# Kernel optimization log

Measured on AMD Instinct MI355X. Metric: run time of the kernel, lower is better.

The kernel has to match this reference:

```python
import jax, jax.numpy as jnp
import numpy as np

DIM = 512
HEADS = 8
HEAD_DIM = DIM // HEADS
SCALE = HEAD_DIM ** -0.5
EPS = 1e-5


def _layernorm(x, w, b):
    mu = jnp.mean(x, axis=-1, keepdims=True)
    var = jnp.mean(jnp.square(x - mu), axis=-1, keepdims=True)
    return (x - mu) * jax.lax.rsqrt(var + EPS) * w + b


def setup_inputs() -> dict:
    key = jax.random.key(0)
    ks = jax.random.split(key, 9)
    B, Hs, Ws = 8, 32, 32
    r = jax.random.normal(ks[0], (B, DIM, Hs, Ws), dtype=jnp.float32)
    z = jax.random.normal(ks[1], (B, DIM, Hs, Ws), dtype=jnp.float32)
    w = lambda k: jax.random.normal(k, (DIM, DIM), dtype=jnp.float32) * 0.02
    return {
        "r": r,
        "z": z,
        "norm_r_w": jnp.ones((DIM,), jnp.float32),
        "norm_r_b": jnp.zeros((DIM,), jnp.float32),
        "norm_z_w": jnp.ones((DIM,), jnp.float32),
        "norm_z_b": jnp.zeros((DIM,), jnp.float32),
        "Wq": w(ks[2]),  # [out, in] torch Linear convention, no bias (qkv_bias=False)
        "Wk": w(ks[3]),
        "Wv": w(ks[4]),
        "Wa": w(ks[5]),
        "Wproj": w(ks[6]),
        "bproj": jax.random.normal(ks[7], (DIM,), dtype=jnp.float32) * 0.02,
    }


def reference(r, z, norm_r_w, norm_r_b, norm_z_w, norm_z_b, Wq, Wk, Wv, Wa, Wproj, bproj):
    z_sc = z
    B, C, Hz, Wz = z.shape
    # flatten(2).permute(0,2,1): NCHW -> [B, N, C]
    rf = r.reshape(B, C, -1).transpose(0, 2, 1)  # [B, Nr, C]
    zf = z.reshape(B, C, -1).transpose(0, 2, 1)  # [B, Nz, C]
    Nr, Nz = rf.shape[1], zf.shape[1]

    rf = _layernorm(rf, norm_r_w, norm_r_b)
    zf = _layernorm(zf, norm_z_w, norm_z_b)

    def heads(x, W, N):  # torch Linear: x @ W.T, then split heads -> [B,H,N,D]
        return (x @ W.T).reshape(B, N, HEADS, HEAD_DIM).transpose(0, 2, 1, 3)

    q = heads(rf, Wq, Nr)  # [B,H,Nr,D]
    k = heads(rf, Wk, Nr)  # [B,H,Nr,D]
    v = heads(zf, Wv, Nz)  # [B,H,Nz,D]
    a = heads(zf, Wa, Nz)  # [B,H,Nz,D]

    # stage 1: softmax(k @ a^T) @ v  -> anchor-aggregated values per r-token
    attn1 = jax.nn.softmax(jnp.einsum('bhnd,bhmd->bhnm', k, a) * SCALE, axis=-1)  # [B,H,Nr,Nz]
    v1 = jnp.einsum('bhnm,bhmd->bhnd', attn1, v)  # [B,H,Nr,D]

    # stage 2: softmax(a @ q^T) @ v1 -> outputs aligned with z tokens
    attn2 = jax.nn.softmax(jnp.einsum('bhmd,bhnd->bhmn', a, q) * SCALE, axis=-1)  # [B,H,Nz,Nr]
    out = jnp.einsum('bhmn,bhnd->bhmd', attn2, v1)  # [B,H,Nz,D]

    out = out.transpose(0, 2, 1, 3).reshape(B, Nz, C)
    out = out @ Wproj.T + bproj
    out = out.transpose(0, 2, 1).reshape(B, C, Hz, Wz)
    return out + z_sc
```

## Files before the change

### kernel.cpp

```cpp
#include <hip/hip_runtime.h>
#include <hip/hip_bf16.h>
#include <stdint.h>


using bf16 = __bf16;
typedef __bf16 bf16x4 __attribute__((ext_vector_type(4)));
typedef __bf16 bf16x8 __attribute__((ext_vector_type(8)));
typedef float f32x4 __attribute__((ext_vector_type(4)));
typedef float f32x16 __attribute__((ext_vector_type(16)));

#define DIMC 512
#define NTOK 1024
#define NB 8
#define NH 8
#define HD 64

__device__ __forceinline__ void gload_lds16(const bf16* g, bf16* l) {
  __builtin_amdgcn_global_load_lds((__attribute__((address_space(1))) void*)g,
                                   (__attribute__((address_space(3))) void*)l,
                                   16, 0, 0);
}

__device__ __forceinline__ float bpermf(int srclane, float v) {
  int i = __builtin_amdgcn_ds_bpermute(srclane << 2, __builtin_bit_cast(int, v));
  return __builtin_bit_cast(float, i);
}

__device__ __forceinline__ int pkbf(float lo, float hi) {
  unsigned short a = __builtin_bit_cast(unsigned short, (bf16)lo);
  unsigned short b = __builtin_bit_cast(unsigned short, (bf16)hi);
  return (int)((unsigned)a | ((unsigned)b << 16));
}

__device__ __forceinline__ float fexp2(float x) {
  float r;
  asm("v_exp_f32 %0, %1" : "=v"(r) : "v"(x));
  return r;
}

__global__ __launch_bounds__(256) void k_ln_fused(
    const float* __restrict__ r, const float* __restrict__ z,
    const float* __restrict__ wr, const float* __restrict__ br,
    const float* __restrict__ wz, const float* __restrict__ bz,
    bf16* __restrict__ rf, bf16* __restrict__ zf) {
  __shared__ float sp[4][64], ssq[4][64];
  __shared__ float muS[64], rsS[64];
  __shared__ __align__(16) bf16 T[64 * 72];
  int n0 = blockIdx.x * 64, b = blockIdx.y, tensor = blockIdx.z;
  const float* x   = tensor ? z  : r;
  const float* w   = tensor ? wz : wr;
  const float* bia = tensor ? bz : br;
  bf16* out = tensor ? zf : rf;
  int tid = threadIdx.x;

  {
    int n = tid & 63, grp = tid >> 6;
    const float* xp = x + ((size_t)(b * DIMC + grp * 128)) * NTOK + n0 + n;
    float s = 0.f, ss = 0.f;
#pragma unroll 8
    for (int c = 0; c < 128; ++c) {
      float v = xp[(size_t)c * NTOK];
      s += v; ss += v * v;
    }
    sp[grp][n] = s; ssq[grp][n] = ss;
  }
  __syncthreads();
  if (tid < 64) {
    float s  = sp[0][tid] + sp[1][tid] + sp[2][tid] + sp[3][tid];
    float ss = ssq[0][tid] + ssq[1][tid] + ssq[2][tid] + ssq[3][tid];
    float m = s * (1.0f / DIMC);
    muS[tid] = m;
    rsS[tid] = rsqrtf(ss * (1.0f / DIMC) - m * m + 1e-5f);
  }
  __syncthreads();

  int cl = tid >> 3;
  int nl = (tid & 7) * 8;
  for (int cs = 0; cs < 8; ++cs) {
    int c0 = cs * 64;
#pragma unroll
    for (int pass = 0; pass < 2; ++pass) {
      int c = c0 + pass * 32 + cl;
      float wc = w[c], bc = bia[c];
      const float* src = x + ((size_t)(b * DIMC + c)) * NTOK + n0 + nl;
      float4 v0 = *reinterpret_cast<const float4*>(src);
      float4 v1 = *reinterpret_cast<const float4*>(src + 4);
      float vv[8] = {v0.x, v0.y, v0.z, v0.w, v1.x, v1.y, v1.z, v1.w};
#pragma unroll
      for (int j = 0; j < 8; ++j) {
        int n = nl + j;
        float val = (vv[j] - muS[n]) * rsS[n] * wc + bc;
        T[n * 72 + pass * 32 + cl] = (bf16)val;
      }
    }
    __syncthreads();
#pragma unroll
    for (int pass = 0; pass < 2; ++pass) {
      int n = pass * 32 + cl;
      bf16x8 o;
#pragma unroll
      for (int j = 0; j < 8; ++j) o[j] = T[n * 72 + nl + j];
      *reinterpret_cast<bf16x8*>(out + ((size_t)(b * NTOK + n0 + n)) * DIMC + c0 + nl) = o;
    }
    __syncthreads();
  }
}

__global__ __launch_bounds__(256) void k_cvt5(
    const float* __restrict__ W0, const float* __restrict__ W1,
    const float* __restrict__ W2, const float* __restrict__ W3,
    const float* __restrict__ W4, bf16* __restrict__ out) {
  int m = blockIdx.y;
  const float* W = (m == 0) ? W0 : (m == 1) ? W1 : (m == 2) ? W2 : (m == 3) ? W3 : W4;
  bf16* o = out + (size_t)m * DIMC * DIMC;
  int i = blockIdx.x * 256 + threadIdx.x;
  float4 v = reinterpret_cast<const float4*>(W)[i];
  bf16x4 b;
  b[0] = (bf16)v.x; b[1] = (bf16)v.y; b[2] = (bf16)v.z; b[3] = (bf16)v.w;
  *reinterpret_cast<bf16x4*>(o + (size_t)i * 4) = b;
}

template <int MODE>
__global__ __launch_bounds__(256) void k_gemm(
    const bf16* __restrict__ actA, const bf16* __restrict__ zf,
    const bf16* __restrict__ Wbf,
    void* __restrict__ outbase,
    const float* __restrict__ zres, const float* __restrict__ bproj) {
  __shared__ __align__(16) bf16 As[128 * 32];
  __shared__ __align__(16) bf16 Bs[128 * 32];
  int b = blockIdx.z;
  const bf16 *Ap, *Bp;
  int m0, n0;
  int mat = (MODE == 0) ? blockIdx.y : -1;
  if (MODE == 0 && mat < 3) {
    Ap = (mat < 2 ? actA : zf) + (size_t)b * NTOK * DIMC;
    int widx = (mat == 2) ? 3 : mat;
    Bp = Wbf + (size_t)widx * DIMC * DIMC;
    m0 = (blockIdx.x >> 2) * 128;
    n0 = (blockIdx.x & 3) * 128;
  } else {
    Ap = Wbf + (size_t)(MODE == 1 ? 4 : 2) * DIMC * DIMC;
    Bp = (MODE == 1 ? actA : zf) + (size_t)b * NTOK * DIMC;
    m0 = (blockIdx.x >> 3) * 128;
    n0 = (blockIdx.x & 7) * 128;
  }
  int tid = threadIdx.x;
  int w = tid >> 6, l = tid & 63;
  int wm = (w >> 1) * 64, wn = (w & 1) * 64;
  int lr = l & 15, lg = l >> 4;
  int srow = l >> 2;
  int scol = (l & 3) * 8;
  f32x4 acc[4][4] = {};

  for (int kt = 0; kt < 16; ++kt) {
    int k0 = kt * 32;
#pragma unroll
    for (int q = 0; q < 2; ++q) {
      int rowA = w * 32 + q * 16 + srow;
      gload_lds16(Ap + (size_t)(m0 + rowA) * DIMC + k0 + scol, &As[(w * 32 + q * 16) * 32]);
      gload_lds16(Bp + (size_t)(n0 + rowA) * DIMC + k0 + scol, &Bs[(w * 32 + q * 16) * 32]);
    }
    __syncthreads();
    bf16x8 af[4], bfr[4];
#pragma unroll
    for (int i = 0; i < 4; ++i)
      af[i] = *reinterpret_cast<const bf16x8*>(&As[(wm + 16 * i + lr) * 32 + lg * 8]);
#pragma unroll
    for (int j = 0; j < 4; ++j)
      bfr[j] = *reinterpret_cast<const bf16x8*>(&Bs[(wn + 16 * j + lr) * 32 + lg * 8]);
#pragma unroll
    for (int i = 0; i < 4; ++i)
#pragma unroll
      for (int j = 0; j < 4; ++j)
        acc[i][j] = __builtin_amdgcn_mfma_f32_16x16x32_bf16(af[i], bfr[j], acc[i][j], 0, 0, 0);
    __syncthreads();
  }

  const size_t SLOT = (size_t)NB * NH * NTOK * HD;
#pragma unroll
  for (int i = 0; i < 4; ++i) {
#pragma unroll
    for (int j = 0; j < 4; ++j) {
#pragma unroll
      for (int rr = 0; rr < 4; ++rr) {
        int mm = m0 + wm + 16 * i + lg * 4 + rr;
        int nn = n0 + wn + 16 * j + lr;
        if (MODE == 0 && mat < 3) {
          bf16* outp = (bf16*)outbase + (size_t)mat * SLOT + (size_t)b * (NH * NTOK * HD);
          outp[((size_t)((nn >> 6) * NTOK + mm)) * HD + (nn & 63)] = (bf16)acc[i][j][rr];
        } else if (MODE == 0) {
          bf16* outp = (bf16*)outbase + 3 * SLOT + (size_t)b * DIMC * NTOK;
          outp[(size_t)mm * NTOK + nn] = (bf16)acc[i][j][rr];
        } else {
          float* outp = (float*)outbase + (size_t)b * DIMC * NTOK;
          const float* zp = zres + (size_t)b * DIMC * NTOK;
          size_t idx = (size_t)mm * NTOK + nn;
          outp[idx] = acc[i][j][rr] + bproj[mm] + zp[idx];
        }
      }
    }
  }
}

__global__ __launch_bounds__(128) void k_flash7(
    const bf16* __restrict__ Qp, const bf16* __restrict__ Kp,
    const bf16* __restrict__ Vtp, bf16* __restrict__ Op, int out_mode) {
  __shared__ __align__(16) bf16 smem[16384];
  int tid = threadIdx.x;
  int w = tid >> 6, l = tid & 63;
  int hl = l >> 5, ln31 = l & 31;
  int id = blockIdx.x;
  int qt = (id >> 3) & 15;
  int bh = ((id & 7) << 3) | (id >> 7);
  int q0 = qt * 64;
  const bf16* Qb = Qp + (size_t)bh * NTOK * HD;
  const bf16* Kb = Kp + (size_t)bh * NTOK * HD;
  const bf16* Vb = Vtp + (size_t)bh * HD * NTOK;

  const float QS = 0.125f * 1.44269504088896340736f;
  bf16x8 qf[4];
  int qrow = q0 + w * 32 + ln31;
#pragma unroll
  for (int s = 0; s < 4; ++s) {
    bf16x8 raw = *reinterpret_cast<const bf16x8*>(Qb + (size_t)qrow * 64 + 16 * s + 8 * hl);
#pragma unroll
    for (int j = 0; j < 8; ++j) qf[s][j] = (bf16)((float)raw[j] * QS);
  }

  int fco = hl * 512 + ln31 * 8;

#pragma unroll
  for (int gg = 0; gg < 4; ++gg) {
    int g = 4 * w + gg;
    int koff = (g >> 1) * 16 + (g & 1) * 8;
    gload_lds16(Kb + (size_t)l * 64 + koff, &smem[g * 512]);
    gload_lds16(Vb + (size_t)l * 1024 + koff, &smem[4096 + g * 512]);
  }

  float l_run = 0.f;
  f32x16 of0{}, of1{};

#pragma unroll 1
  for (int kt = 0; kt < 16; ++kt) {
    __syncthreads();
    int buf = (kt & 1) ? 8192 : 0;

    if (kt + 1 < 16) {
      int k0n = (kt + 1) * 64;
      int nb = buf ^ 8192;
#pragma unroll
      for (int gg = 0; gg < 4; ++gg) {
        int g = 4 * w + gg;
        int koff = (g >> 1) * 16 + (g & 1) * 8;
        gload_lds16(Kb + (size_t)(k0n + l) * 64 + koff, &smem[nb + g * 512]);
        gload_lds16(Vb + (size_t)l * 1024 + k0n + koff, &smem[nb + 4096 + g * 512]);
      }
    }

    const bf16* Ks = &smem[buf];
    const bf16* Vs = &smem[buf + 4096];

    bf16x8 kf0[4], kf1[4];
#pragma unroll
    for (int s = 0; s < 4; ++s) {
      kf0[s] = *reinterpret_cast<const bf16x8*>(&Ks[s * 1024 + fco]);
      kf1[s] = *reinterpret_cast<const bf16x8*>(&Ks[s * 1024 + fco + 256]);
    }

    f32x16 sT0, sT1;
#pragma unroll
    for (int r = 0; r < 16; ++r) { sT0[r] = -16.0f; sT1[r] = -16.0f; }
    __builtin_amdgcn_s_setprio(1);
#pragma unroll
    for (int s = 0; s < 4; ++s) {
      sT0 = __builtin_amdgcn_mfma_f32_32x32x16_bf16(kf0[s], qf[s], sT0, 0, 0, 0);
      sT1 = __builtin_amdgcn_mfma_f32_32x32x16_bf16(kf1[s], qf[s], sT1, 0, 0, 0);
    }
    __builtin_amdgcn_s_setprio(0);

    float s0 = 0.f, s1 = 0.f, s2 = 0.f, s3 = 0.f;
#pragma unroll
    for (int r = 0; r < 16; r += 4) {
      sT0[r]     = fexp2(sT0[r]);     s0 += sT0[r];
      sT0[r + 1] = fexp2(sT0[r + 1]); s1 += sT0[r + 1];
      sT0[r + 2] = fexp2(sT0[r + 2]); s2 += sT0[r + 2];
      sT0[r + 3] = fexp2(sT0[r + 3]); s3 += sT0[r + 3];
      sT1[r]     = fexp2(sT1[r]);     s0 += sT1[r];
      sT1[r + 1] = fexp2(sT1[r + 1]); s1 += sT1[r + 1];
      sT1[r + 2] = fexp2(sT1[r + 2]); s2 += sT1[r + 2];
      sT1[r + 3] = fexp2(sT1[r + 3]); s3 += sT1[r + 3];
    }
    l_run += (s0 + s1) + (s2 + s3);

    bf16x8 vf0[4], vf1[4];
#pragma unroll
    for (int ks = 0; ks < 4; ++ks) {
      vf0[ks] = *reinterpret_cast<const bf16x8*>(&Vs[ks * 1024 + fco]);
      vf1[ks] = *reinterpret_cast<const bf16x8*>(&Vs[ks * 1024 + fco + 256]);
    }

    int wpk[16];
#pragma unroll
    for (int g = 0; g < 4; ++g) {
      wpk[2 * g]     = pkbf(sT0[4 * g],     sT0[4 * g + 1]);
      wpk[2 * g + 1] = pkbf(sT0[4 * g + 2], sT0[4 * g + 3]);
      wpk[2 * (g + 4)]     = pkbf(sT1[4 * g],     sT1[4 * g + 1]);
      wpk[2 * (g + 4) + 1] = pkbf(sT1[4 * g + 2], sT1[4 * g + 3]);
    }
    int rw[16];
#pragma unroll
    for (int t = 0; t < 16; ++t) rw[t] = __shfl_xor(wpk[t], 32);

    bf16x8 pf[4];
#pragma unroll
    for (int ks = 0; ks < 4; ++ks) {
      int gA = 2 * ks, gB = 2 * ks + 1;
      union { int i[4]; bf16x8 v; } u;
      u.i[0] = hl ? rw[2 * gB]     : wpk[2 * gA];
      u.i[1] = hl ? rw[2 * gB + 1] : wpk[2 * gA + 1];
      u.i[2] = hl ? wpk[2 * gB]     : rw[2 * gA];
      u.i[3] = hl ? wpk[2 * gB + 1] : rw[2 * gA + 1];
      pf[ks] = u.v;
    }

    __builtin_amdgcn_s_setprio(1);
#pragma unroll
    for (int ks = 0; ks < 4; ++ks) {
      of0 = __builtin_amdgcn_mfma_f32_32x32x16_bf16(pf[ks], vf0[ks], of0, 0, 0, 0);
      of1 = __builtin_amdgcn_mfma_f32_32x32x16_bf16(pf[ks], vf1[ks], of1, 0, 0, 0);
    }
    __builtin_amdgcn_s_setprio(0);
  }

  __syncthreads();
  float lt = l_run + __shfl_xor(l_run, 32);
  float inv = 1.0f / lt;
  if (out_mode == 0) {
    bf16* T = &smem[w * 2560];
#pragma unroll
    for (int r = 0; r < 16; ++r) {
      int qloc = (r & 3) + 8 * (r >> 2) + 4 * hl;
      float invr = bpermf(qloc + (l & 32), inv);
      T[ln31 * 40 + qloc] = (bf16)(of0[r] * invr);
      T[(ln31 + 32) * 40 + qloc] = (bf16)(of1[r] * invr);
    }
#pragma unroll
    for (int i = 0; i < 4; ++i) {
      int d = (l >> 2) + 16 * i;
      int qc = (l & 3) * 8;
      bf16x8 v = *reinterpret_cast<const bf16x8*>(&T[d * 40 + qc]);
      *reinterpret_cast<bf16x8*>(Op + ((size_t)bh * HD + d) * NTOK + q0 + w * 32 + qc) = v;
    }
  } else {
#pragma unroll
    for (int r = 0; r < 16; ++r) {
      int qloc = (r & 3) + 8 * (r >> 2) + 4 * hl;
      float invr = bpermf(qloc + (l & 32), inv);
      int q = q0 + w * 32 + qloc;
      int b = bh >> 3, h = bh & 7;
      bf16* p = Op + ((size_t)(b * NTOK + q)) * DIMC + h * 64;
      p[ln31] = (bf16)(of0[r] * invr);
      p[ln31 + 32] = (bf16)(of1[r] * invr);
    }
  }
}

extern "C" void kernel_launch(void* const* d_in, const int* in_sizes, int n_in,
                              void* d_out, int out_size, void* d_ws, size_t ws_size,
                              hipStream_t stream) {
  const float* r  = (const float*)d_in[0];
  const float* z  = (const float*)d_in[1];
  const float* wr = (const float*)d_in[2];
  const float* br = (const float*)d_in[3];
  const float* wz = (const float*)d_in[4];
  const float* bz = (const float*)d_in[5];
  const float* Wq = (const float*)d_in[6];
  const float* Wk = (const float*)d_in[7];
  const float* Wv = (const float*)d_in[8];
  const float* Wa = (const float*)d_in[9];
  const float* Wp = (const float*)d_in[10];
  const float* bp = (const float*)d_in[11];

  char* ws = (char*)d_ws;
  bf16* rf   = (bf16*)ws;
  bf16* zf   = rf + (size_t)NB * NTOK * DIMC;
  bf16* qka  = zf + (size_t)NB * NTOK * DIMC;
  const size_t SLOT = (size_t)NB * NH * NTOK * HD;
  bf16* vt  = qka + 3 * SLOT;
  bf16* v1t = qka + 4 * SLOT;
  bf16* at2 = v1t + SLOT;
  bf16* Wbf = at2 + SLOT;

  bf16* Qt = qka;
  bf16* Kt = qka + 1 * SLOT;
  bf16* At = qka + 2 * SLOT;

  k_ln_fused<<<dim3(16, NB, 2), 256, 0, stream>>>(r, z, wr, br, wz, bz, rf, zf);
  k_cvt5<<<dim3(256, 5), 256, 0, stream>>>(Wq, Wk, Wv, Wa, Wp, Wbf);
  k_gemm<0><<<dim3(32, 4, NB), 256, 0, stream>>>(rf, zf, Wbf, qka, nullptr, nullptr);
  k_flash7<<<1024, 128, 0, stream>>>(Kt, At, vt, v1t, 0);
  k_flash7<<<1024, 128, 0, stream>>>(At, Qt, v1t, at2, 1);
  k_gemm<1><<<dim3(32, 1, NB), 256, 0, stream>>>(at2, nullptr, Wbf, d_out, z, bp);
}
```

Measured before the change: 152.3 us.

## Split attention KV range across blocks and merge partials in combine kernel

The flash attention kernel now uses 256-thread blocks covering 128 query rows, and each block processes only half of the key/value sequence. Unnormalized partial outputs and row sums go to scratch buffers, and a new combine kernel adds the two halves, normalizes, and writes the transposed or head-interleaved layout. This doubles query rows per block so each K/V tile is reused across more queries. It also gives each block more waves to hide latency. The cost is extra global traffic for the partials and two additional kernel launches, and it relies on the fixed softmax offset so the partials can simply be summed.

After: 150.0 us. Within noise of the previous version (-1.5%).

```diff
diff --git a/kernel.cpp b/kernel.cpp
--- a/kernel.cpp
+++ b/kernel.cpp
@@ -19,11 +19,6 @@
   __builtin_amdgcn_global_load_lds((__attribute__((address_space(1))) void*)g,
                                    (__attribute__((address_space(3))) void*)l,
                                    16, 0, 0);
-}
-
-__device__ __forceinline__ float bpermf(int srclane, float v) {
-  int i = __builtin_amdgcn_ds_bpermute(srclane << 2, __builtin_bit_cast(int, v));
-  return __builtin_bit_cast(float, i);
 }
 
 __device__ __forceinline__ int pkbf(float lo, float hi) {
@@ -202,20 +197,25 @@
   }
 }
 
-__global__ __launch_bounds__(128) void k_flash7(
+__global__ __launch_bounds__(256) void k_flash8(
     const bf16* __restrict__ Qp, const bf16* __restrict__ Kp,
-    const bf16* __restrict__ Vtp, bf16* __restrict__ Op, int out_mode) {
+    const bf16* __restrict__ Vtp, bf16* __restrict__ P0, bf16* __restrict__ P1,
+    float* __restrict__ lbuf) {
   __shared__ __align__(16) bf16 smem[16384];
   int tid = threadIdx.x;
   int w = tid >> 6, l = tid & 63;
   int hl = l >> 5, ln31 = l & 31;
   int id = blockIdx.x;
-  int qt = (id >> 3) & 15;
+  int qt = (id >> 3) & 7;
+  int kvh = (id >> 6) & 1;
   int bh = ((id & 7) << 3) | (id >> 7);
-  int q0 = qt * 64;
+  int q0 = qt * 128;
+  int kbase = kvh * 512;
   const bf16* Qb = Qp + (size_t)bh * NTOK * HD;
   const bf16* Kb = Kp + (size_t)bh * NTOK * HD;
   const bf16* Vb = Vtp + (size_t)bh * HD * NTOK;
+  bf16* Pp = (kvh ? P1 : P0) + ((size_t)bh * NTOK + q0 + w * 32) * HD;
+  float* lp = lbuf + (size_t)kvh * (64 * NTOK) + (size_t)bh * NTOK + q0 + w * 32;
 
   const float QS = 0.125f * 1.44269504088896340736f;
   bf16x8 qf[4];
@@ -227,34 +227,30 @@
     for (int j = 0; j < 8; ++j) qf[s][j] = (bf16)((float)raw[j] * QS);
   }
 
+  int koff0 = w * 16;
+  int koff1 = w * 16 + 8;
   int fco = hl * 512 + ln31 * 8;
 
-#pragma unroll
-  for (int gg = 0; gg < 4; ++gg) {
-    int g = 4 * w + gg;
-    int koff = (g >> 1) * 16 + (g & 1) * 8;
-    gload_lds16(Kb + (size_t)l * 64 + koff, &smem[g * 512]);
-    gload_lds16(Vb + (size_t)l * 1024 + koff, &smem[4096 + g * 512]);
-  }
+  gload_lds16(Kb + (size_t)(kbase + l) * 64 + koff0, &smem[(2 * w) * 512]);
+  gload_lds16(Kb + (size_t)(kbase + l) * 64 + koff1, &smem[(2 * w + 1) * 512]);
+  gload_lds16(Vb + (size_t)l * 1024 + kbase + koff0, &smem[4096 + (2 * w) * 512]);
+  gload_lds16(Vb + (size_t)l * 1024 + kbase + koff1, &smem[4096 + (2 * w + 1) * 512]);
 
   float l_run = 0.f;
   f32x16 of0{}, of1{};
 
 #pragma unroll 1
-  for (int kt = 0; kt < 16; ++kt) {
+  for (int kt = 0; kt < 8; ++kt) {
     __syncthreads();
     int buf = (kt & 1) ? 8192 : 0;
 
-    if (kt + 1 < 16) {
-      int k0n = (kt + 1) * 64;
+    if (kt + 1 < 8) {
+      int k0n = kbase + (kt + 1) * 64;
       int nb = buf ^ 8192;
-#pragma unroll
-      for (int gg = 0; gg < 4; ++gg) {
-        int g = 4 * w + gg;
-        int koff = (g >> 1) * 16 + (g & 1) * 8;
-        gload_lds16(Kb + (size_t)(k0n + l) * 64 + koff, &smem[nb + g * 512]);
-        gload_lds16(Vb + (size_t)l * 1024 + k0n + koff, &smem[nb + 4096 + g * 512]);
-      }
+      gload_lds16(Kb + (size_t)(k0n + l) * 64 + koff0, &smem[nb + (2 * w) * 512]);
+      gload_lds16(Kb + (size_t)(k0n + l) * 64 + koff1, &smem[nb + (2 * w + 1) * 512]);
+      gload_lds16(Vb + (size_t)l * 1024 + k0n + koff0, &smem[nb + 4096 + (2 * w) * 512]);
+      gload_lds16(Vb + (size_t)l * 1024 + k0n + koff1, &smem[nb + 4096 + (2 * w + 1) * 512]);
     }
 
     const bf16* Ks = &smem[buf];
@@ -332,35 +328,57 @@
     __builtin_amdgcn_s_setprio(0);
   }
 
-  __syncthreads();
   float lt = l_run + __shfl_xor(l_run, 32);
-  float inv = 1.0f / lt;
+  if (hl == 0) lp[ln31] = lt;
+#pragma unroll
+  for (int r = 0; r < 16; ++r) {
+    int qloc = (r & 3) + 8 * (r >> 2) + 4 * hl;
+    bf16* p = Pp + (size_t)qloc * HD;
+    p[ln31] = (bf16)of0[r];
+    p[ln31 + 32] = (bf16)of1[r];
+  }
+}
+
+__global__ __launch_bounds__(256) void k_combine(
+    const bf16* __restrict__ P0, const bf16* __restrict__ P1,
+    const float* __restrict__ lbuf, bf16* __restrict__ Out, int out_mode) {
+  __shared__ __align__(16) bf16 T[64 * 72];
+  int nt = blockIdx.x, bh = blockIdx.y;
+  int tid = threadIdx.x;
+  const bf16* P0b = P0 + ((size_t)bh * NTOK + nt * 64) * HD;
+  const bf16* P1b = P1 + ((size_t)bh * NTOK + nt * 64) * HD;
+  const float* l0 = lbuf + (size_t)bh * NTOK + nt * 64;
+  const float* l1 = l0 + (size_t)64 * NTOK;
+  int nr = tid >> 3;
+  int d0 = (tid & 7) * 8;
+
+#pragma unroll
+  for (int pass = 0; pass < 2; ++pass) {
+    int n = pass * 32 + nr;
+    float inv = 1.0f / (l0[n] + l1[n]);
+    bf16x8 a = *reinterpret_cast<const bf16x8*>(P0b + (size_t)n * HD + d0);
+    bf16x8 b = *reinterpret_cast<const bf16x8*>(P1b + (size_t)n * HD + d0);
+    bf16x8 o;
+#pragma unroll
+    for (int j = 0; j < 8; ++j) o[j] = (bf16)(((float)a[j] + (float)b[j]) * inv);
+    if (out_mode == 1) {
+      int b_ = bh >> 3, h = bh & 7;
+      *reinterpret_cast<bf16x8*>(Out + ((size_t)(b_ * NTOK + nt * 64 + n)) * DIMC + h * HD + d0) = o;
+    } else {
+#pragma unroll
+      for (int j = 0; j < 8; ++j) T[n * 72 + d0 + j] = o[j];
+    }
+  }
   if (out_mode == 0) {
-    bf16* T = &smem[w * 2560];
-#pragma unroll
-    for (int r = 0; r < 16; ++r) {
-      int qloc = (r & 3) + 8 * (r >> 2) + 4 * hl;
-      float invr = bpermf(qloc + (l & 32), inv);
-      T[ln31 * 40 + qloc] = (bf16)(of0[r] * invr);
-      T[(ln31 + 32) * 40 + qloc] = (bf16)(of1[r] * invr);
-    }
-#pragma unroll
-    for (int i = 0; i < 4; ++i) {
-      int d = (l >> 2) + 16 * i;
-      int qc = (l & 3) * 8;
-      bf16x8 v = *reinterpret_cast<const bf16x8*>(&T[d * 40 + qc]);
-      *reinterpret_cast<bf16x8*>(Op + ((size_t)bh * HD + d) * NTOK + q0 + w * 32 + qc) = v;
-    }
-  } else {
-#pragma unroll
-    for (int r = 0; r < 16; ++r) {
-      int qloc = (r & 3) + 8 * (r >> 2) + 4 * hl;
-      float invr = bpermf(qloc + (l & 32), inv);
-      int q = q0 + w * 32 + qloc;
-      int b = bh >> 3, h = bh & 7;
-      bf16* p = Op + ((size_t)(b * NTOK + q)) * DIMC + h * 64;
-      p[ln31] = (bf16)(of0[r] * invr);
-      p[ln31 + 32] = (bf16)(of1[r] * invr);
+    __syncthreads();
+#pragma unroll
+    for (int pass = 0; pass < 2; ++pass) {
+      int d = pass * 32 + nr;
+      int nc = d0;
+      bf16x8 o;
+#pragma unroll
+      for (int j = 0; j < 8; ++j) o[j] = T[(nc + j) * 72 + d];
+      *reinterpret_cast<bf16x8*>(Out + ((size_t)bh * HD + d) * NTOK + nt * 64 + nc) = o;
     }
   }
 }
@@ -395,10 +413,17 @@
   bf16* Kt = qka + 1 * SLOT;
   bf16* At = qka + 2 * SLOT;
 
+  bf16* Pa = rf;
+  bf16* Pb = zf;
+  float* lbuf1 = (float*)at2;
+  float* lbuf2 = (float*)Kt;
+
   k_ln_fused<<<dim3(16, NB, 2), 256, 0, stream>>>(r, z, wr, br, wz, bz, rf, zf);
   k_cvt5<<<dim3(256, 5), 256, 0, stream>>>(Wq, Wk, Wv, Wa, Wp, Wbf);
   k_gemm<0><<<dim3(32, 4, NB), 256, 0, stream>>>(rf, zf, Wbf, qka, nullptr, nullptr);
-  k_flash7<<<1024, 128, 0, stream>>>(Kt, At, vt, v1t, 0);
-  k_flash7<<<1024, 128, 0, stream>>>(At, Qt, v1t, at2, 1);
+  k_flash8<<<1024, 256, 0, stream>>>(Kt, At, vt, Pa, Pb, lbuf1);
+  k_combine<<<dim3(16, 64), 256, 0, stream>>>(Pa, Pb, lbuf1, v1t, 0);
+  k_flash8<<<1024, 256, 0, stream>>>(At, Qt, v1t, Pa, Pb, lbuf2);
+  k_combine<<<dim3(16, 64), 256, 0, stream>>>(Pa, Pb, lbuf2, at2, 1);
   k_gemm<1><<<dim3(32, 1, NB), 256, 0, stream>>>(at2, nullptr, Wbf, d_out, z, bp);
 }
```

## Widen flash query tile to 4 waves and double GEMM K-step

Applied to the files above, without the earlier changes.

The attention kernel now runs 4 waves per block over 128 query rows, so each K/V tile staged in LDS serves twice as many queries. Each wave issues half as many async loads, and the grid is halved. The P-fragment cross-half exchange now shuffles only the half-rows needed, cutting shuffle count. The projection GEMMs load a 64-wide K slab per barrier pair, halving synchronisation count at the cost of doubled LDS use.

New measurement: 135.5 us. -11.0%, faster.

```diff
diff --git a/kernel.cpp b/kernel.cpp
--- a/kernel.cpp
+++ b/kernel.cpp
@@ -126,8 +126,8 @@
     const bf16* __restrict__ Wbf,
     void* __restrict__ outbase,
     const float* __restrict__ zres, const float* __restrict__ bproj) {
-  __shared__ __align__(16) bf16 As[128 * 32];
-  __shared__ __align__(16) bf16 Bs[128 * 32];
+  __shared__ __align__(16) bf16 As[2 * 128 * 32];
+  __shared__ __align__(16) bf16 Bs[2 * 128 * 32];
   int b = blockIdx.z;
   const bf16 *Ap, *Bp;
   int m0, n0;
@@ -152,27 +152,35 @@
   int scol = (l & 3) * 8;
   f32x4 acc[4][4] = {};
 
-  for (int kt = 0; kt < 16; ++kt) {
-    int k0 = kt * 32;
-#pragma unroll
-    for (int q = 0; q < 2; ++q) {
-      int rowA = w * 32 + q * 16 + srow;
-      gload_lds16(Ap + (size_t)(m0 + rowA) * DIMC + k0 + scol, &As[(w * 32 + q * 16) * 32]);
-      gload_lds16(Bp + (size_t)(n0 + rowA) * DIMC + k0 + scol, &Bs[(w * 32 + q * 16) * 32]);
+  for (int kt = 0; kt < 8; ++kt) {
+    int k0 = kt * 64;
+#pragma unroll
+    for (int s = 0; s < 2; ++s) {
+#pragma unroll
+      for (int q = 0; q < 2; ++q) {
+        int rowA = w * 32 + q * 16 + srow;
+        gload_lds16(Ap + (size_t)(m0 + rowA) * DIMC + k0 + s * 32 + scol,
+                    &As[s * 4096 + (w * 32 + q * 16) * 32]);
+        gload_lds16(Bp + (size_t)(n0 + rowA) * DIMC + k0 + s * 32 + scol,
+                    &Bs[s * 4096 + (w * 32 + q * 16) * 32]);
+      }
     }
     __syncthreads();
-    bf16x8 af[4], bfr[4];
-#pragma unroll
-    for (int i = 0; i < 4; ++i)
-      af[i] = *reinterpret_cast<const bf16x8*>(&As[(wm + 16 * i + lr) * 32 + lg * 8]);
-#pragma unroll
-    for (int j = 0; j < 4; ++j)
-      bfr[j] = *reinterpret_cast<const bf16x8*>(&Bs[(wn + 16 * j + lr) * 32 + lg * 8]);
-#pragma unroll
-    for (int i = 0; i < 4; ++i)
+#pragma unroll
+    for (int s = 0; s < 2; ++s) {
+      bf16x8 af[4], bfr[4];
+#pragma unroll
+      for (int i = 0; i < 4; ++i)
+        af[i] = *reinterpret_cast<const bf16x8*>(&As[s * 4096 + (wm + 16 * i + lr) * 32 + lg * 8]);
 #pragma unroll
       for (int j = 0; j < 4; ++j)
-        acc[i][j] = __builtin_amdgcn_mfma_f32_16x16x32_bf16(af[i], bfr[j], acc[i][j], 0, 0, 0);
+        bfr[j] = *reinterpret_cast<const bf16x8*>(&Bs[s * 4096 + (wn + 16 * j + lr) * 32 + lg * 8]);
+#pragma unroll
+      for (int i = 0; i < 4; ++i)
+#pragma unroll
+        for (int j = 0; j < 4; ++j)
+          acc[i][j] = __builtin_amdgcn_mfma_f32_16x16x32_bf16(af[i], bfr[j], acc[i][j], 0, 0, 0);
+    }
     __syncthreads();
   }
 
@@ -202,7 +210,7 @@
   }
 }
 
-__global__ __launch_bounds__(128) void k_flash7(
+__global__ __launch_bounds__(256) void k_flash9(
     const bf16* __restrict__ Qp, const bf16* __restrict__ Kp,
     const bf16* __restrict__ Vtp, bf16* __restrict__ Op, int out_mode) {
   __shared__ __align__(16) bf16 smem[16384];
@@ -210,9 +218,9 @@
   int w = tid >> 6, l = tid & 63;
   int hl = l >> 5, ln31 = l & 31;
   int id = blockIdx.x;
-  int qt = (id >> 3) & 15;
-  int bh = ((id & 7) << 3) | (id >> 7);
-  int q0 = qt * 64;
+  int qt = (id >> 3) & 7;
+  int bh = ((id & 7) << 3) | (id >> 6);
+  int q0 = qt * 128;
   const bf16* Qb = Qp + (size_t)bh * NTOK * HD;
   const bf16* Kb = Kp + (size_t)bh * NTOK * HD;
   const bf16* Vb = Vtp + (size_t)bh * HD * NTOK;
@@ -227,15 +235,14 @@
     for (int j = 0; j < 8; ++j) qf[s][j] = (bf16)((float)raw[j] * QS);
   }
 
+  int koff0 = w * 16;
+  int koff1 = w * 16 + 8;
   int fco = hl * 512 + ln31 * 8;
 
-#pragma unroll
-  for (int gg = 0; gg < 4; ++gg) {
-    int g = 4 * w + gg;
-    int koff = (g >> 1) * 16 + (g & 1) * 8;
-    gload_lds16(Kb + (size_t)l * 64 + koff, &smem[g * 512]);
-    gload_lds16(Vb + (size_t)l * 1024 + koff, &smem[4096 + g * 512]);
-  }
+  gload_lds16(Kb + (size_t)l * 64 + koff0, &smem[(2 * w) * 512]);
+  gload_lds16(Kb + (size_t)l * 64 + koff1, &smem[(2 * w + 1) * 512]);
+  gload_lds16(Vb + (size_t)l * 1024 + koff0, &smem[4096 + (2 * w) * 512]);
+  gload_lds16(Vb + (size_t)l * 1024 + koff1, &smem[4096 + (2 * w + 1) * 512]);
 
   float l_run = 0.f;
   f32x16 of0{}, of1{};
@@ -248,13 +255,10 @@
     if (kt + 1 < 16) {
       int k0n = (kt + 1) * 64;
       int nb = buf ^ 8192;
-#pragma unroll
-      for (int gg = 0; gg < 4; ++gg) {
-        int g = 4 * w + gg;
-        int koff = (g >> 1) * 16 + (g & 1) * 8;
-        gload_lds16(Kb + (size_t)(k0n + l) * 64 + koff, &smem[nb + g * 512]);
-        gload_lds16(Vb + (size_t)l * 1024 + k0n + koff, &smem[nb + 4096 + g * 512]);
-      }
+      gload_lds16(Kb + (size_t)(k0n + l) * 64 + koff0, &smem[nb + (2 * w) * 512]);
+      gload_lds16(Kb + (size_t)(k0n + l) * 64 + koff1, &smem[nb + (2 * w + 1) * 512]);
+      gload_lds16(Vb + (size_t)l * 1024 + k0n + koff0, &smem[nb + 4096 + (2 * w) * 512]);
+      gload_lds16(Vb + (size_t)l * 1024 + k0n + koff1, &smem[nb + 4096 + (2 * w + 1) * 512]);
     }
 
     const bf16* Ks = &smem[buf];
@@ -307,19 +311,19 @@
       wpk[2 * (g + 4)]     = pkbf(sT1[4 * g],     sT1[4 * g + 1]);
       wpk[2 * (g + 4) + 1] = pkbf(sT1[4 * g + 2], sT1[4 * g + 3]);
     }
-    int rw[16];
-#pragma unroll
-    for (int t = 0; t < 16; ++t) rw[t] = __shfl_xor(wpk[t], 32);
 
     bf16x8 pf[4];
 #pragma unroll
     for (int ks = 0; ks < 4; ++ks) {
-      int gA = 2 * ks, gB = 2 * ks + 1;
+      int send0 = hl ? wpk[4 * ks]     : wpk[4 * ks + 2];
+      int send1 = hl ? wpk[4 * ks + 1] : wpk[4 * ks + 3];
+      int recv0 = __shfl_xor(send0, 32);
+      int recv1 = __shfl_xor(send1, 32);
       union { int i[4]; bf16x8 v; } u;
-      u.i[0] = hl ? rw[2 * gB]     : wpk[2 * gA];
-      u.i[1] = hl ? rw[2 * gB + 1] : wpk[2 * gA + 1];
-      u.i[2] = hl ? wpk[2 * gB]     : rw[2 * gA];
-      u.i[3] = hl ? wpk[2 * gB + 1] : rw[2 * gA + 1];
+      u.i[0] = hl ? recv0 : wpk[4 * ks];
+      u.i[1] = hl ? recv1 : wpk[4 * ks + 1];
+      u.i[2] = hl ? wpk[4 * ks + 2] : recv0;
+      u.i[3] = hl ? wpk[4 * ks + 3] : recv1;
       pf[ks] = u.v;
     }
 
@@ -386,7 +390,6 @@
   bf16* zf   = rf + (size_t)NB * NTOK * DIMC;
   bf16* qka  = zf + (size_t)NB * NTOK * DIMC;
   const size_t SLOT = (size_t)NB * NH * NTOK * HD;
-  bf16* vt  = qka + 3 * SLOT;
   bf16* v1t = qka + 4 * SLOT;
   bf16* at2 = v1t + SLOT;
   bf16* Wbf = at2 + SLOT;
@@ -394,11 +397,12 @@
   bf16* Qt = qka;
   bf16* Kt = qka + 1 * SLOT;
   bf16* At = qka + 2 * SLOT;
+  bf16* vt = qka + 3 * SLOT;
 
   k_ln_fused<<<dim3(16, NB, 2), 256, 0, stream>>>(r, z, wr, br, wz, bz, rf, zf);
   k_cvt5<<<dim3(256, 5), 256, 0, stream>>>(Wq, Wk, Wv, Wa, Wp, Wbf);
   k_gemm<0><<<dim3(32, 4, NB), 256, 0, stream>>>(rf, zf, Wbf, qka, nullptr, nullptr);
-  k_flash7<<<1024, 128, 0, stream>>>(Kt, At, vt, v1t, 0);
-  k_flash7<<<1024, 128, 0, stream>>>(At, Qt, v1t, at2, 1);
+  k_flash9<<<512, 256, 0, stream>>>(Kt, At, vt, v1t, 0);
+  k_flash9<<<512, 256, 0, stream>>>(At, Qt, v1t, at2, 1);
   k_gemm<1><<<dim3(32, 1, NB), 256, 0, stream>>>(at2, nullptr, Wbf, d_out, z, bp);
 }
```
